# Kernel optimization log

Hardware: AMD Instinct MI355X
Metric: run time of the kernel (lower is better)

The kernel has to match this reference:

```python
import jax, jax.numpy as jnp
import numpy as np

D_MODEL = 2048
N_STATE = 256          # power of two
RANK = 64
LEVELS = int(np.log2(N_STATE))  # 8 butterfly levels
B, S = 4, 4096


def setup_inputs() -> dict:
    key = jax.random.key(0)
    ks = jax.random.split(key, 7)
    u = jax.random.normal(ks[0], (B, S, D_MODEL), dtype=jnp.float32)
    # stacked 2x2 butterfly factors, one per level (orthogonal-ish init)
    A_factors = jax.random.normal(ks[1], (LEVELS, 2, 2), dtype=jnp.float32)
    A_factors = A_factors / jnp.linalg.norm(A_factors, axis=-1, keepdims=True)
    W_b_rank = jax.random.normal(ks[2], (D_MODEL, RANK), dtype=jnp.float32) * (1.0 / np.sqrt(D_MODEL))
    W_b_state = jax.random.normal(ks[3], (RANK, N_STATE), dtype=jnp.float32) * (1.0 / np.sqrt(RANK))
    W_c_rank = jax.random.normal(ks[4], (N_STATE, RANK), dtype=jnp.float32) * (1.0 / np.sqrt(N_STATE))
    W_c_model = jax.random.normal(ks[5], (RANK, D_MODEL), dtype=jnp.float32) * (1.0 / np.sqrt(RANK))
    D_vec = jax.random.normal(ks[6], (D_MODEL,), dtype=jnp.float32) * 0.02
    return {"u": u, "A_factors": A_factors, "W_b_rank": W_b_rank,
            "W_b_state": W_b_state, "W_c_rank": W_c_rank,
            "W_c_model": W_c_model, "D_vec": D_vec}


def _apply_butterfly(state, A_factors):
    # state: [B, S, N]; reshape N into LEVELS axes of size 2 and apply a 2x2
    # factor along each axis (contracting the axis with A's FIRST dim, i.e.
    # x @ A, matching tf.matmul(flattened, factor)).
    b, s, n = state.shape
    x = state.reshape((b, s) + (2,) * LEVELS)
    for lvl in range(LEVELS):
        ax = 2 + lvl
        x = jnp.moveaxis(jnp.tensordot(x, A_factors[lvl], axes=[[ax], [0]]), -1, ax)
    return x.reshape(b, s, n)


def reference(u, A_factors, W_b_rank, W_b_state, W_c_rank, W_c_model, D_vec):
    # B path: low-rank projection to state space
    state = (u @ W_b_rank) @ W_b_state              # [B,S,N]
    # A: butterfly-structured state transform
    state = _apply_butterfly(state, A_factors)      # [B,S,N]
    # C path: low-rank projection back to model dim
    y = (state @ W_c_rank) @ W_c_model              # [B,S,D]
    # D: elementwise feedthrough
    return y + D_vec * u
```

## Files before the change

### kernel.cpp

```cpp
#include <hip/hip_runtime.h>

typedef unsigned short ushort_t;
typedef __attribute__((ext_vector_type(8))) short bf16x8;
typedef __attribute__((ext_vector_type(4))) float f32x4;
typedef __attribute__((ext_vector_type(4))) unsigned short us4;

#define DM 2048
#define RK 64

__device__ __forceinline__ ushort_t f2b(float f) {
    union { float f; unsigned u; } x; x.f = f;
    unsigned r = x.u + 0x7fff + ((x.u >> 16) & 1);
    return (ushort_t)(r >> 16);
}

__global__ void k_p1(const float* __restrict__ Wbs, const float* __restrict__ Af,
                     const float* __restrict__ Wcr, float* __restrict__ Mmid) {
    __shared__ float X[64 * 256];
    const int tid = threadIdx.x;

#pragma unroll
    for (int i = 0; i < 16; ++i) {
        int e = (i * 256 + tid) * 4;
        *(float4*)&X[e] = *(const float4*)&Wbs[e];
    }
    __syncthreads();

#pragma unroll
    for (int l = 0; l < 8; ++l) {
        const int bit = 1 << (7 - l);
        const float a00 = Af[l * 4 + 0], a01 = Af[l * 4 + 1];
        const float a10 = Af[l * 4 + 2], a11 = Af[l * 4 + 3];
#pragma unroll 4
        for (int p = 0; p < 32; ++p) {
            int pid = p * 256 + tid;
            int row = pid >> 7;
            int off = pid & 127;
            int lo = off & (bit - 1);
            int n0 = ((off ^ lo) << 1) | lo;
            int n1 = n0 | bit;
            float x0 = X[row * 256 + n0], x1 = X[row * 256 + n1];
            X[row * 256 + n0] = x0 * a00 + x1 * a10;
            X[row * 256 + n1] = x0 * a01 + x1 * a11;
        }
        __syncthreads();
    }

    int g = blockIdx.x * 256 + tid;
    int r1 = g >> 6, r2 = g & 63;
    float s = 0.f;
#pragma unroll 8
    for (int n = 0; n < 256; ++n) s += X[r1 * 256 + n] * Wcr[n * 64 + r2];
    Mmid[g] = s;
}

__global__ void k_p2(const float* __restrict__ Wbr, const float* __restrict__ Mmid,
                     const float* __restrict__ Wcm,
                     ushort_t* __restrict__ WeffT, ushort_t* __restrict__ WcT) {
    const int b = blockIdx.x, tid = threadIdx.x;
    if (b < 32) {
        __shared__ float LW[64][65];
        __shared__ float LM[64 * 64];
#pragma unroll
        for (int i = 0; i < 4; ++i) {
            int e = (i * 256 + tid) * 4;
            int kk = e >> 6, r = e & 63;
            float4 v = *(const float4*)&Wbr[(size_t)b * 4096 + e];
            LW[kk][r] = v.x; LW[kk][r + 1] = v.y; LW[kk][r + 2] = v.z; LW[kk][r + 3] = v.w;
        }
#pragma unroll
        for (int i = 0; i < 4; ++i) {
            int e = (i * 256 + tid) * 4;
            *(float4*)&LM[e] = *(const float4*)&Mmid[e];
        }
        __syncthreads();

        int kk = tid & 63, n0 = (tid >> 6) * 16;
        float acc[16];
#pragma unroll
        for (int j = 0; j < 16; ++j) acc[j] = 0.f;
        for (int r = 0; r < 64; ++r) {
            float wv = LW[kk][r];
            const float* mrow = &LM[r * 64 + n0];
            float4 m0 = *(const float4*)(mrow);
            float4 m1 = *(const float4*)(mrow + 4);
            float4 m2 = *(const float4*)(mrow + 8);
            float4 m3 = *(const float4*)(mrow + 12);
            acc[0] += wv * m0.x; acc[1] += wv * m0.y; acc[2] += wv * m0.z; acc[3] += wv * m0.w;
            acc[4] += wv * m1.x; acc[5] += wv * m1.y; acc[6] += wv * m1.z; acc[7] += wv * m1.w;
            acc[8] += wv * m2.x; acc[9] += wv * m2.y; acc[10] += wv * m2.z; acc[11] += wv * m2.w;
            acc[12] += wv * m3.x; acc[13] += wv * m3.y; acc[14] += wv * m3.z; acc[15] += wv * m3.w;
        }
#pragma unroll
        for (int j = 0; j < 16; ++j)
            WeffT[(size_t)(n0 + j) * DM + b * 64 + kk] = f2b(acc[j]);
    } else {
        __shared__ float LT[64][65];
        const int n0 = (b - 32) * 64;
#pragma unroll
        for (int i = 0; i < 4; ++i) {
            int e = (i * 256 + tid) * 4;
            int k = e >> 6, nn = e & 63;
            float4 v = *(const float4*)&Wcm[(size_t)k * DM + n0 + nn];
            LT[k][nn] = v.x; LT[k][nn + 1] = v.y; LT[k][nn + 2] = v.z; LT[k][nn + 3] = v.w;
        }
        __syncthreads();
#pragma unroll
        for (int i = 0; i < 4; ++i) {
            int e = (i * 256 + tid) * 4;
            int nn = e >> 6, k = e & 63;
            us4 o;
            o.x = f2b(LT[k][nn]); o.y = f2b(LT[k + 1][nn]);
            o.z = f2b(LT[k + 2][nn]); o.w = f2b(LT[k + 3][nn]);
            *(us4*)&WcT[(size_t)(n0 + nn) * RK + k] = o;
        }
    }
}

__global__ __launch_bounds__(512, 5) void k_main(const float* __restrict__ u,
                                                 const ushort_t* __restrict__ WeffT,
                                                 const ushort_t* __restrict__ WcT,
                                                 const float* __restrict__ Dvec,
                                                 float* __restrict__ out) {
    __shared__ float red[8][64][20];
    __shared__ ushort_t tsh[16 * 72];

    const int tid = threadIdx.x;
    const int w = tid >> 6;
    const int lane = tid & 63;
    const int m16 = lane & 15;
    const int quad = lane >> 4;
    const size_t row0 = (size_t)blockIdx.x * 16;
    const float* ub = u + row0 * DM;

    f32x4 acc0 = {0.f, 0.f, 0.f, 0.f}, acc1 = acc0, acc2 = acc0, acc3 = acc0;
    const float* ap = ub + m16 * DM + w * 256 + quad * 8;
    const ushort_t* bp0 = WeffT + (size_t)m16 * DM + w * 256 + quad * 8;
#pragma unroll 4
    for (int ks = 0; ks < 8; ++ks) {
        const int k0 = ks * 32;
        float4 u0 = *(const float4*)(ap + k0);
        float4 u1 = *(const float4*)(ap + k0 + 4);
        bf16x8 a;
        a[0] = (short)f2b(u0.x); a[1] = (short)f2b(u0.y);
        a[2] = (short)f2b(u0.z); a[3] = (short)f2b(u0.w);
        a[4] = (short)f2b(u1.x); a[5] = (short)f2b(u1.y);
        a[6] = (short)f2b(u1.z); a[7] = (short)f2b(u1.w);
        bf16x8 b0 = *(const bf16x8*)(bp0 + k0);
        bf16x8 b1 = *(const bf16x8*)(bp0 + 16 * DM + k0);
        bf16x8 b2 = *(const bf16x8*)(bp0 + 32 * DM + k0);
        bf16x8 b3 = *(const bf16x8*)(bp0 + 48 * DM + k0);
        acc0 = __builtin_amdgcn_mfma_f32_16x16x32_bf16(a, b0, acc0, 0, 0, 0);
        acc1 = __builtin_amdgcn_mfma_f32_16x16x32_bf16(a, b1, acc1, 0, 0, 0);
        acc2 = __builtin_amdgcn_mfma_f32_16x16x32_bf16(a, b2, acc2, 0, 0, 0);
        acc3 = __builtin_amdgcn_mfma_f32_16x16x32_bf16(a, b3, acc3, 0, 0, 0);
    }
    *(f32x4*)&red[w][ 0 + m16][quad * 4] = acc0;
    *(f32x4*)&red[w][16 + m16][quad * 4] = acc1;
    *(f32x4*)&red[w][32 + m16][quad * 4] = acc2;
    *(f32x4*)&red[w][48 + m16][quad * 4] = acc3;
    __syncthreads();

    {
        const int n = tid >> 3, r2 = (tid & 7) * 2;
        float s0 = 0.f, s1 = 0.f;
#pragma unroll
        for (int ww = 0; ww < 8; ++ww) {
            float2 v = *(const float2*)&red[ww][n][r2];
            s0 += v.x; s1 += v.y;
        }
        tsh[r2 * 72 + n]       = f2b(s0);
        tsh[(r2 + 1) * 72 + n] = f2b(s1);
    }
    __syncthreads();

    bf16x8 ta0 = *(const bf16x8*)&tsh[m16 * 72 + quad * 8];
    bf16x8 ta1 = *(const bf16x8*)&tsh[m16 * 72 + 32 + quad * 8];
    const ushort_t* wcb = WcT + (size_t)(w * 256 + m16) * RK + quad * 8;
    const float* u2 = ub + m16 * DM + w * 256 + quad * 4;
    const float* dp = Dvec + w * 256 + quad * 4;
    float* op = out + (row0 + m16) * DM + w * 256 + quad * 4;
#pragma unroll 2
    for (int nt = 0; nt < 16; ++nt) {
        const ushort_t* bp2 = wcb + nt * 16 * RK;
        bf16x8 wb0 = *(const bf16x8*)(bp2);
        bf16x8 wb1 = *(const bf16x8*)(bp2 + 32);
        f32x4 o = {0.f, 0.f, 0.f, 0.f};
        o = __builtin_amdgcn_mfma_f32_16x16x32_bf16(wb0, ta0, o, 0, 0, 0);
        o = __builtin_amdgcn_mfma_f32_16x16x32_bf16(wb1, ta1, o, 0, 0, 0);
        float4 uv = *(const float4*)(u2 + nt * 16);
        float4 dv = *(const float4*)(dp + nt * 16);
        f32x4 st;
        st.x = o[0] + dv.x * uv.x;
        st.y = o[1] + dv.y * uv.y;
        st.z = o[2] + dv.z * uv.z;
        st.w = o[3] + dv.w * uv.w;
        __builtin_nontemporal_store(st, (f32x4*)(op + nt * 16));
    }
}

extern "C" void kernel_launch(void* const* d_in, const int* in_sizes, int n_in,
                              void* d_out, int out_size, void* d_ws, size_t ws_size,
                              hipStream_t stream) {
    (void)in_sizes; (void)n_in; (void)out_size; (void)ws_size;
    const float* u   = (const float*)d_in[0];
    const float* Af  = (const float*)d_in[1];
    const float* Wbr = (const float*)d_in[2];
    const float* Wbs = (const float*)d_in[3];
    const float* Wcr = (const float*)d_in[4];
    const float* Wcm = (const float*)d_in[5];
    const float* Dv  = (const float*)d_in[6];
    float* out = (float*)d_out;

    char* ws = (char*)d_ws;
    float*    Mmid  = (float*)(ws + 0);
    ushort_t* WeffT = (ushort_t*)(ws + 16384);
    ushort_t* WcT   = (ushort_t*)(ws + 278528);

    k_p1<<<16, 256, 0, stream>>>(Wbs, Af, Wcr, Mmid);
    k_p2<<<64, 256, 0, stream>>>(Wbr, Mmid, Wcm, WeffT, WcT);
    k_main<<<1024, 512, 0, stream>>>(u, WeffT, WcT, Dv, out);
}
```

Before: 327.2 us.

## Split fused main kernel into separate reduce and expand kernels

Splits the fused k_main into two launches. k_a uses 128-thread blocks, each warp covering half of K, and writes the rank-64 intermediate for each 16-row block to global memory as bf16. k_b uses 256-thread blocks that read that intermediate and do the output projection plus the D feedthrough. The aim is to drop the 8-way shared-memory reduction and the large-block occupancy limit. In exchange, u is read twice across two kernels, there is an extra launch, and a global round-trip for the intermediate.

New measurement: 323.1 us. About the same (-1.2%).

```diff
diff --git a/kernel.cpp b/kernel.cpp
--- a/kernel.cpp
+++ b/kernel.cpp
@@ -18,14 +18,12 @@
                      const float* __restrict__ Wcr, float* __restrict__ Mmid) {
     __shared__ float X[64 * 256];
     const int tid = threadIdx.x;
-
 #pragma unroll
     for (int i = 0; i < 16; ++i) {
         int e = (i * 256 + tid) * 4;
         *(float4*)&X[e] = *(const float4*)&Wbs[e];
     }
     __syncthreads();
-
 #pragma unroll
     for (int l = 0; l < 8; ++l) {
         const int bit = 1 << (7 - l);
@@ -45,7 +43,6 @@
         }
         __syncthreads();
     }
-
     int g = blockIdx.x * 256 + tid;
     int r1 = g >> 6, r2 = g & 63;
     float s = 0.f;
@@ -74,7 +71,6 @@
             *(float4*)&LM[e] = *(const float4*)&Mmid[e];
         }
         __syncthreads();
-
         int kk = tid & 63, n0 = (tid >> 6) * 16;
         float acc[16];
 #pragma unroll
@@ -117,28 +113,23 @@
     }
 }
 
-__global__ __launch_bounds__(512, 5) void k_main(const float* __restrict__ u,
-                                                 const ushort_t* __restrict__ WeffT,
-                                                 const ushort_t* __restrict__ WcT,
-                                                 const float* __restrict__ Dvec,
-                                                 float* __restrict__ out) {
-    __shared__ float red[8][64][20];
-    __shared__ ushort_t tsh[16 * 72];
-
+__global__ __launch_bounds__(128) void k_a(const float* __restrict__ u,
+                                           const ushort_t* __restrict__ WeffT,
+                                           ushort_t* __restrict__ tg) {
+    __shared__ float red[2][16][68];
     const int tid = threadIdx.x;
     const int w = tid >> 6;
     const int lane = tid & 63;
     const int m16 = lane & 15;
     const int quad = lane >> 4;
     const size_t row0 = (size_t)blockIdx.x * 16;
-    const float* ub = u + row0 * DM;
+    const float* ap = u + (row0 + m16) * DM + w * 1024 + quad * 8;
+    const ushort_t* bp0 = WeffT + (size_t)m16 * DM + w * 1024 + quad * 8;
 
     f32x4 acc0 = {0.f, 0.f, 0.f, 0.f}, acc1 = acc0, acc2 = acc0, acc3 = acc0;
-    const float* ap = ub + m16 * DM + w * 256 + quad * 8;
-    const ushort_t* bp0 = WeffT + (size_t)m16 * DM + w * 256 + quad * 8;
 #pragma unroll 4
-    for (int ks = 0; ks < 8; ++ks) {
-        const int k0 = ks * 32;
+    for (int kk = 0; kk < 32; ++kk) {
+        const int k0 = kk * 32;
         float4 u0 = *(const float4*)(ap + k0);
         float4 u1 = *(const float4*)(ap + k0 + 4);
         bf16x8 a;
@@ -155,33 +146,53 @@
         acc2 = __builtin_amdgcn_mfma_f32_16x16x32_bf16(a, b2, acc2, 0, 0, 0);
         acc3 = __builtin_amdgcn_mfma_f32_16x16x32_bf16(a, b3, acc3, 0, 0, 0);
     }
-    *(f32x4*)&red[w][ 0 + m16][quad * 4] = acc0;
-    *(f32x4*)&red[w][16 + m16][quad * 4] = acc1;
-    *(f32x4*)&red[w][32 + m16][quad * 4] = acc2;
-    *(f32x4*)&red[w][48 + m16][quad * 4] = acc3;
+#pragma unroll
+    for (int i = 0; i < 4; ++i) {
+        red[w][quad * 4 + i][ 0 + m16] = acc0[i];
+        red[w][quad * 4 + i][16 + m16] = acc1[i];
+        red[w][quad * 4 + i][32 + m16] = acc2[i];
+        red[w][quad * 4 + i][48 + m16] = acc3[i];
+    }
     __syncthreads();
 
     {
-        const int n = tid >> 3, r2 = (tid & 7) * 2;
-        float s0 = 0.f, s1 = 0.f;
-#pragma unroll
-        for (int ww = 0; ww < 8; ++ww) {
-            float2 v = *(const float2*)&red[ww][n][r2];
-            s0 += v.x; s1 += v.y;
-        }
-        tsh[r2 * 72 + n]       = f2b(s0);
-        tsh[(r2 + 1) * 72 + n] = f2b(s1);
-    }
-    __syncthreads();
-
-    bf16x8 ta0 = *(const bf16x8*)&tsh[m16 * 72 + quad * 8];
-    bf16x8 ta1 = *(const bf16x8*)&tsh[m16 * 72 + 32 + quad * 8];
-    const ushort_t* wcb = WcT + (size_t)(w * 256 + m16) * RK + quad * 8;
-    const float* u2 = ub + m16 * DM + w * 256 + quad * 4;
-    const float* dp = Dvec + w * 256 + quad * 4;
-    float* op = out + (row0 + m16) * DM + w * 256 + quad * 4;
+        const int row = tid >> 3, c0 = (tid & 7) * 8;
+        float4 p0 = *(const float4*)&red[0][row][c0];
+        float4 p1 = *(const float4*)&red[0][row][c0 + 4];
+        float4 q0 = *(const float4*)&red[1][row][c0];
+        float4 q1 = *(const float4*)&red[1][row][c0 + 4];
+        us4 o0, o1;
+        o0.x = f2b(p0.x + q0.x); o0.y = f2b(p0.y + q0.y);
+        o0.z = f2b(p0.z + q0.z); o0.w = f2b(p0.w + q0.w);
+        o1.x = f2b(p1.x + q1.x); o1.y = f2b(p1.y + q1.y);
+        o1.z = f2b(p1.z + q1.z); o1.w = f2b(p1.w + q1.w);
+        ushort_t* tp = tg + (size_t)blockIdx.x * 1024 + tid * 8;
+        *(us4*)tp = o0;
+        *(us4*)(tp + 4) = o1;
+    }
+}
+
+__global__ __launch_bounds__(256) void k_b(const ushort_t* __restrict__ tg,
+                                           const float* __restrict__ u,
+                                           const ushort_t* __restrict__ WcT,
+                                           const float* __restrict__ Dvec,
+                                           float* __restrict__ out) {
+    const int tid = threadIdx.x;
+    const int w = tid >> 6;
+    const int lane = tid & 63;
+    const int m16 = lane & 15;
+    const int quad = lane >> 4;
+    const size_t row0 = (size_t)blockIdx.x * 16;
+    const ushort_t* tb = tg + (size_t)blockIdx.x * 1024;
+
+    bf16x8 ta0 = *(const bf16x8*)&tb[m16 * 64 + quad * 8];
+    bf16x8 ta1 = *(const bf16x8*)&tb[m16 * 64 + 32 + quad * 8];
+    const ushort_t* wcb = WcT + (size_t)(w * 512 + m16) * RK + quad * 8;
+    const float* u2 = u + (row0 + m16) * DM + w * 512 + quad * 4;
+    const float* dp = Dvec + w * 512 + quad * 4;
+    float* op = out + (row0 + m16) * DM + w * 512 + quad * 4;
 #pragma unroll 2
-    for (int nt = 0; nt < 16; ++nt) {
+    for (int nt = 0; nt < 32; ++nt) {
         const ushort_t* bp2 = wcb + nt * 16 * RK;
         bf16x8 wb0 = *(const bf16x8*)(bp2);
         bf16x8 wb1 = *(const bf16x8*)(bp2 + 32);
@@ -216,8 +227,10 @@
     float*    Mmid  = (float*)(ws + 0);
     ushort_t* WeffT = (ushort_t*)(ws + 16384);
     ushort_t* WcT   = (ushort_t*)(ws + 278528);
+    ushort_t* tg    = (ushort_t*)(ws + 540672);
 
     k_p1<<<16, 256, 0, stream>>>(Wbs, Af, Wcr, Mmid);
     k_p2<<<64, 256, 0, stream>>>(Wbr, Mmid, Wcm, WeffT, WcT);
-    k_main<<<1024, 512, 0, stream>>>(u, WeffT, WcT, Dv, out);
-}
+    k_a <<<1024, 128, 0, stream>>>(u, WeffT, tg);
+    k_b <<<1024, 256, 0, stream>>>(tg, u, WcT, Dv, out);
+}
```

## Use 4-wave blocks with software-prefetched loads in main fused kernel

Applied to the files above, without the earlier changes.

Halves the block size of the main kernel from 8 to 4 waves, so each wave covers a 512-wide K slice (16 MFMA steps) and a 512-wide output slice. Both loops gain explicit register double-buffering that issues the next iteration's global loads before the current MFMAs. The cross-wave reduction buffer is laid out transposed so the reduction reads contiguous float4 rows. The aim is to hide global-load latency and cut reduction traffic, at the cost of more registers per thread and fewer waves per block to hide latency.

Result: slower. 354.8 us (+8.4%).

```diff
diff --git a/kernel.cpp b/kernel.cpp
--- a/kernel.cpp
+++ b/kernel.cpp
@@ -18,14 +18,12 @@
                      const float* __restrict__ Wcr, float* __restrict__ Mmid) {
     __shared__ float X[64 * 256];
     const int tid = threadIdx.x;
-
 #pragma unroll
     for (int i = 0; i < 16; ++i) {
         int e = (i * 256 + tid) * 4;
         *(float4*)&X[e] = *(const float4*)&Wbs[e];
     }
     __syncthreads();
-
 #pragma unroll
     for (int l = 0; l < 8; ++l) {
         const int bit = 1 << (7 - l);
@@ -45,7 +43,6 @@
         }
         __syncthreads();
     }
-
     int g = blockIdx.x * 256 + tid;
     int r1 = g >> 6, r2 = g & 63;
     float s = 0.f;
@@ -74,7 +71,6 @@
             *(float4*)&LM[e] = *(const float4*)&Mmid[e];
         }
         __syncthreads();
-
         int kk = tid & 63, n0 = (tid >> 6) * 16;
         float acc[16];
 #pragma unroll
@@ -117,12 +113,12 @@
     }
 }
 
-__global__ __launch_bounds__(512, 5) void k_main(const float* __restrict__ u,
+__global__ __launch_bounds__(256, 4) void k_main(const float* __restrict__ u,
                                                  const ushort_t* __restrict__ WeffT,
                                                  const ushort_t* __restrict__ WcT,
                                                  const float* __restrict__ Dvec,
                                                  float* __restrict__ out) {
-    __shared__ float red[8][64][20];
+    __shared__ float red[4][16][68];
     __shared__ ushort_t tsh[16 * 72];
 
     const int tid = threadIdx.x;
@@ -133,69 +129,99 @@
     const size_t row0 = (size_t)blockIdx.x * 16;
     const float* ub = u + row0 * DM;
 
+    const float* ap = ub + m16 * DM + w * 512 + quad * 8;
+    const ushort_t* bp = WeffT + (size_t)m16 * DM + w * 512 + quad * 8;
+
     f32x4 acc0 = {0.f, 0.f, 0.f, 0.f}, acc1 = acc0, acc2 = acc0, acc3 = acc0;
-    const float* ap = ub + m16 * DM + w * 256 + quad * 8;
-    const ushort_t* bp0 = WeffT + (size_t)m16 * DM + w * 256 + quad * 8;
-#pragma unroll 4
-    for (int ks = 0; ks < 8; ++ks) {
-        const int k0 = ks * 32;
-        float4 u0 = *(const float4*)(ap + k0);
-        float4 u1 = *(const float4*)(ap + k0 + 4);
+    float4 u0c = *(const float4*)(ap);
+    float4 u1c = *(const float4*)(ap + 4);
+    bf16x8 b0c = *(const bf16x8*)(bp);
+    bf16x8 b1c = *(const bf16x8*)(bp + 16 * DM);
+    bf16x8 b2c = *(const bf16x8*)(bp + 32 * DM);
+    bf16x8 b3c = *(const bf16x8*)(bp + 48 * DM);
+#pragma unroll
+    for (int kk = 0; kk < 16; ++kk) {
+        float4 u0n, u1n; bf16x8 b0n, b1n, b2n, b3n;
+        if (kk < 15) {
+            const int k0 = (kk + 1) * 32;
+            u0n = *(const float4*)(ap + k0);
+            u1n = *(const float4*)(ap + k0 + 4);
+            b0n = *(const bf16x8*)(bp + k0);
+            b1n = *(const bf16x8*)(bp + 16 * DM + k0);
+            b2n = *(const bf16x8*)(bp + 32 * DM + k0);
+            b3n = *(const bf16x8*)(bp + 48 * DM + k0);
+        }
         bf16x8 a;
-        a[0] = (short)f2b(u0.x); a[1] = (short)f2b(u0.y);
-        a[2] = (short)f2b(u0.z); a[3] = (short)f2b(u0.w);
-        a[4] = (short)f2b(u1.x); a[5] = (short)f2b(u1.y);
-        a[6] = (short)f2b(u1.z); a[7] = (short)f2b(u1.w);
-        bf16x8 b0 = *(const bf16x8*)(bp0 + k0);
-        bf16x8 b1 = *(const bf16x8*)(bp0 + 16 * DM + k0);
-        bf16x8 b2 = *(const bf16x8*)(bp0 + 32 * DM + k0);
-        bf16x8 b3 = *(const bf16x8*)(bp0 + 48 * DM + k0);
-        acc0 = __builtin_amdgcn_mfma_f32_16x16x32_bf16(a, b0, acc0, 0, 0, 0);
-        acc1 = __builtin_amdgcn_mfma_f32_16x16x32_bf16(a, b1, acc1, 0, 0, 0);
-        acc2 = __builtin_amdgcn_mfma_f32_16x16x32_bf16(a, b2, acc2, 0, 0, 0);
-        acc3 = __builtin_amdgcn_mfma_f32_16x16x32_bf16(a, b3, acc3, 0, 0, 0);
-    }
-    *(f32x4*)&red[w][ 0 + m16][quad * 4] = acc0;
-    *(f32x4*)&red[w][16 + m16][quad * 4] = acc1;
-    *(f32x4*)&red[w][32 + m16][quad * 4] = acc2;
-    *(f32x4*)&red[w][48 + m16][quad * 4] = acc3;
+        a[0] = (short)f2b(u0c.x); a[1] = (short)f2b(u0c.y);
+        a[2] = (short)f2b(u0c.z); a[3] = (short)f2b(u0c.w);
+        a[4] = (short)f2b(u1c.x); a[5] = (short)f2b(u1c.y);
+        a[6] = (short)f2b(u1c.z); a[7] = (short)f2b(u1c.w);
+        acc0 = __builtin_amdgcn_mfma_f32_16x16x32_bf16(a, b0c, acc0, 0, 0, 0);
+        acc1 = __builtin_amdgcn_mfma_f32_16x16x32_bf16(a, b1c, acc1, 0, 0, 0);
+        acc2 = __builtin_amdgcn_mfma_f32_16x16x32_bf16(a, b2c, acc2, 0, 0, 0);
+        acc3 = __builtin_amdgcn_mfma_f32_16x16x32_bf16(a, b3c, acc3, 0, 0, 0);
+        if (kk < 15) {
+            u0c = u0n; u1c = u1n;
+            b0c = b0n; b1c = b1n; b2c = b2n; b3c = b3n;
+        }
+    }
+#pragma unroll
+    for (int i = 0; i < 4; ++i) {
+        red[w][quad * 4 + i][ 0 + m16] = acc0[i];
+        red[w][quad * 4 + i][16 + m16] = acc1[i];
+        red[w][quad * 4 + i][32 + m16] = acc2[i];
+        red[w][quad * 4 + i][48 + m16] = acc3[i];
+    }
     __syncthreads();
 
     {
-        const int n = tid >> 3, r2 = (tid & 7) * 2;
-        float s0 = 0.f, s1 = 0.f;
-#pragma unroll
-        for (int ww = 0; ww < 8; ++ww) {
-            float2 v = *(const float2*)&red[ww][n][r2];
-            s0 += v.x; s1 += v.y;
-        }
-        tsh[r2 * 72 + n]       = f2b(s0);
-        tsh[(r2 + 1) * 72 + n] = f2b(s1);
+        const int row = tid >> 4, c0 = (tid & 15) * 4;
+        float4 s0 = *(const float4*)&red[0][row][c0];
+        float4 s1 = *(const float4*)&red[1][row][c0];
+        float4 s2 = *(const float4*)&red[2][row][c0];
+        float4 s3 = *(const float4*)&red[3][row][c0];
+        us4 o;
+        o.x = f2b(s0.x + s1.x + s2.x + s3.x);
+        o.y = f2b(s0.y + s1.y + s2.y + s3.y);
+        o.z = f2b(s0.z + s1.z + s2.z + s3.z);
+        o.w = f2b(s0.w + s1.w + s2.w + s3.w);
+        *(us4*)&tsh[row * 72 + c0] = o;
     }
     __syncthreads();
 
     bf16x8 ta0 = *(const bf16x8*)&tsh[m16 * 72 + quad * 8];
     bf16x8 ta1 = *(const bf16x8*)&tsh[m16 * 72 + 32 + quad * 8];
-    const ushort_t* wcb = WcT + (size_t)(w * 256 + m16) * RK + quad * 8;
-    const float* u2 = ub + m16 * DM + w * 256 + quad * 4;
-    const float* dp = Dvec + w * 256 + quad * 4;
-    float* op = out + (row0 + m16) * DM + w * 256 + quad * 4;
-#pragma unroll 2
-    for (int nt = 0; nt < 16; ++nt) {
-        const ushort_t* bp2 = wcb + nt * 16 * RK;
-        bf16x8 wb0 = *(const bf16x8*)(bp2);
-        bf16x8 wb1 = *(const bf16x8*)(bp2 + 32);
+    const ushort_t* wcb = WcT + (size_t)(w * 512 + m16) * RK + quad * 8;
+    const float* u2 = ub + m16 * DM + w * 512 + quad * 4;
+    const float* dp = Dvec + w * 512 + quad * 4;
+    float* op = out + (row0 + m16) * DM + w * 512 + quad * 4;
+
+    bf16x8 wb0c = *(const bf16x8*)(wcb);
+    bf16x8 wb1c = *(const bf16x8*)(wcb + 32);
+    float4 uvc = *(const float4*)(u2);
+    float4 dvc = *(const float4*)(dp);
+#pragma unroll 4
+    for (int nt = 0; nt < 32; ++nt) {
+        bf16x8 wb0n, wb1n; float4 uvn, dvn;
+        if (nt < 31) {
+            const ushort_t* bp2 = wcb + (nt + 1) * 16 * RK;
+            wb0n = *(const bf16x8*)(bp2);
+            wb1n = *(const bf16x8*)(bp2 + 32);
+            uvn = *(const float4*)(u2 + (nt + 1) * 16);
+            dvn = *(const float4*)(dp + (nt + 1) * 16);
+        }
         f32x4 o = {0.f, 0.f, 0.f, 0.f};
-        o = __builtin_amdgcn_mfma_f32_16x16x32_bf16(wb0, ta0, o, 0, 0, 0);
-        o = __builtin_amdgcn_mfma_f32_16x16x32_bf16(wb1, ta1, o, 0, 0, 0);
-        float4 uv = *(const float4*)(u2 + nt * 16);
-        float4 dv = *(const float4*)(dp + nt * 16);
+        o = __builtin_amdgcn_mfma_f32_16x16x32_bf16(wb0c, ta0, o, 0, 0, 0);
+        o = __builtin_amdgcn_mfma_f32_16x16x32_bf16(wb1c, ta1, o, 0, 0, 0);
         f32x4 st;
-        st.x = o[0] + dv.x * uv.x;
-        st.y = o[1] + dv.y * uv.y;
-        st.z = o[2] + dv.z * uv.z;
-        st.w = o[3] + dv.w * uv.w;
+        st.x = o[0] + dvc.x * uvc.x;
+        st.y = o[1] + dvc.y * uvc.y;
+        st.z = o[2] + dvc.z * uvc.z;
+        st.w = o[3] + dvc.w * uvc.w;
         __builtin_nontemporal_store(st, (f32x4*)(op + nt * 16));
+        if (nt < 31) {
+            wb0c = wb0n; wb1c = wb1n; uvc = uvn; dvc = dvn;
+        }
     }
 }
 
@@ -219,5 +245,5 @@
 
     k_p1<<<16, 256, 0, stream>>>(Wbs, Af, Wcr, Mmid);
     k_p2<<<64, 256, 0, stream>>>(Wbr, Mmid, Wcm, WeffT, WcT);
-    k_main<<<1024, 512, 0, stream>>>(u, WeffT, WcT, Dv, out);
-}
+    k_main<<<1024, 256, 0, stream>>>(u, WeffT, WcT, Dv, out);
+}
```

## Restructure main kernel to single-wave blocks with double-buffered LDS staging of u

Applied to the files above, without the earlier changes.

The main kernel now runs one wavefront per 16-row block instead of eight wavefronts splitting the K dimension. Each wave walks the full 2048-wide K in 16 stages. Tiles of u are staged into a swizzled, double-buffered LDS buffer with global_load_lds, and the cross-wave LDS reduction is removed. The goal is to overlap u loads with MFMA work and drop the reduction and barrier cost. In exchange, each CU gets far fewer waves to hide latency, the output epilogue becomes a 128-iteration serial loop in one wave, and the nontemporal store hint is removed. There is no explicit wait between the LDS DMA loads and the LDS reads, so correctness depends on the waits the compiler inserts.

Result: slower. 337.7 us (+3.2%).

```diff
diff --git a/kernel.cpp b/kernel.cpp
--- a/kernel.cpp
+++ b/kernel.cpp
@@ -18,14 +18,12 @@
                      const float* __restrict__ Wcr, float* __restrict__ Mmid) {
     __shared__ float X[64 * 256];
     const int tid = threadIdx.x;
-
 #pragma unroll
     for (int i = 0; i < 16; ++i) {
         int e = (i * 256 + tid) * 4;
         *(float4*)&X[e] = *(const float4*)&Wbs[e];
     }
     __syncthreads();
-
 #pragma unroll
     for (int l = 0; l < 8; ++l) {
         const int bit = 1 << (7 - l);
@@ -45,7 +43,6 @@
         }
         __syncthreads();
     }
-
     int g = blockIdx.x * 256 + tid;
     int r1 = g >> 6, r2 = g & 63;
     float s = 0.f;
@@ -74,7 +71,6 @@
             *(float4*)&LM[e] = *(const float4*)&Mmid[e];
         }
         __syncthreads();
-
         int kk = tid & 63, n0 = (tid >> 6) * 16;
         float acc[16];
 #pragma unroll
@@ -117,72 +113,87 @@
     }
 }
 
-__global__ __launch_bounds__(512, 5) void k_main(const float* __restrict__ u,
-                                                 const ushort_t* __restrict__ WeffT,
-                                                 const ushort_t* __restrict__ WcT,
-                                                 const float* __restrict__ Dvec,
-                                                 float* __restrict__ out) {
-    __shared__ float red[8][64][20];
+__global__ __launch_bounds__(64, 1) void k_main(const float* __restrict__ u,
+                                                const ushort_t* __restrict__ WeffT,
+                                                const ushort_t* __restrict__ WcT,
+                                                const float* __restrict__ Dvec,
+                                                float* __restrict__ out) {
+    __shared__ float sbuf[2][16 * 128];
     __shared__ ushort_t tsh[16 * 72];
 
-    const int tid = threadIdx.x;
-    const int w = tid >> 6;
-    const int lane = tid & 63;
+    const int lane = threadIdx.x;
     const int m16 = lane & 15;
     const int quad = lane >> 4;
     const size_t row0 = (size_t)blockIdx.x * 16;
     const float* ub = u + row0 * DM;
 
+#define STAGE(BUF, S)                                                          \
+    {                                                                          \
+        _Pragma("unroll")                                                      \
+        for (int j = 0; j < 8; ++j) {                                          \
+            int srow = j * 2 + (lane >> 5);                                    \
+            int p = lane & 31;                                                 \
+            int g = p ^ srow ^ ((srow & 2) << 3);                              \
+            const float* gp = ub + (size_t)srow * DM + (S) * 128 + g * 4;      \
+            __builtin_amdgcn_global_load_lds(                                  \
+                (const __attribute__((address_space(1))) void*)gp,             \
+                (__attribute__((address_space(3))) void*)&sbuf[BUF][j * 256],  \
+                16, 0, 0);                                                     \
+        }                                                                      \
+    }
+
     f32x4 acc0 = {0.f, 0.f, 0.f, 0.f}, acc1 = acc0, acc2 = acc0, acc3 = acc0;
-    const float* ap = ub + m16 * DM + w * 256 + quad * 8;
-    const ushort_t* bp0 = WeffT + (size_t)m16 * DM + w * 256 + quad * 8;
-#pragma unroll 4
-    for (int ks = 0; ks < 8; ++ks) {
-        const int k0 = ks * 32;
-        float4 u0 = *(const float4*)(ap + k0);
-        float4 u1 = *(const float4*)(ap + k0 + 4);
-        bf16x8 a;
-        a[0] = (short)f2b(u0.x); a[1] = (short)f2b(u0.y);
-        a[2] = (short)f2b(u0.z); a[3] = (short)f2b(u0.w);
-        a[4] = (short)f2b(u1.x); a[5] = (short)f2b(u1.y);
-        a[6] = (short)f2b(u1.z); a[7] = (short)f2b(u1.w);
-        bf16x8 b0 = *(const bf16x8*)(bp0 + k0);
-        bf16x8 b1 = *(const bf16x8*)(bp0 + 16 * DM + k0);
-        bf16x8 b2 = *(const bf16x8*)(bp0 + 32 * DM + k0);
-        bf16x8 b3 = *(const bf16x8*)(bp0 + 48 * DM + k0);
-        acc0 = __builtin_amdgcn_mfma_f32_16x16x32_bf16(a, b0, acc0, 0, 0, 0);
-        acc1 = __builtin_amdgcn_mfma_f32_16x16x32_bf16(a, b1, acc1, 0, 0, 0);
-        acc2 = __builtin_amdgcn_mfma_f32_16x16x32_bf16(a, b2, acc2, 0, 0, 0);
-        acc3 = __builtin_amdgcn_mfma_f32_16x16x32_bf16(a, b3, acc3, 0, 0, 0);
-    }
-    *(f32x4*)&red[w][ 0 + m16][quad * 4] = acc0;
-    *(f32x4*)&red[w][16 + m16][quad * 4] = acc1;
-    *(f32x4*)&red[w][32 + m16][quad * 4] = acc2;
-    *(f32x4*)&red[w][48 + m16][quad * 4] = acc3;
-    __syncthreads();
-
-    {
-        const int n = tid >> 3, r2 = (tid & 7) * 2;
-        float s0 = 0.f, s1 = 0.f;
-#pragma unroll
-        for (int ww = 0; ww < 8; ++ww) {
-            float2 v = *(const float2*)&red[ww][n][r2];
-            s0 += v.x; s1 += v.y;
-        }
-        tsh[r2 * 72 + n]       = f2b(s0);
-        tsh[(r2 + 1) * 72 + n] = f2b(s1);
+
+    STAGE(0, 0);
+    for (int s = 0; s < 16; ++s) {
+        const int cur = s & 1;
+        bf16x8 wf0[4], wf1[4], wf2[4], wf3[4];
+#pragma unroll
+        for (int ks = 0; ks < 4; ++ks) {
+            const ushort_t* wp = WeffT + (size_t)m16 * DM + s * 128 + ks * 32 + quad * 8;
+            wf0[ks] = *(const bf16x8*)(wp);
+            wf1[ks] = *(const bf16x8*)(wp + 16 * DM);
+            wf2[ks] = *(const bf16x8*)(wp + 32 * DM);
+            wf3[ks] = *(const bf16x8*)(wp + 48 * DM);
+        }
+        if (s < 15) STAGE(cur ^ 1, s + 1);
+
+#pragma unroll
+        for (int ks = 0; ks < 4; ++ks) {
+            const int c0 = ks * 8 + quad * 2;
+            const int swz = m16 ^ ((m16 & 2) << 3);
+            f32x4 va = *(const f32x4*)&sbuf[cur][m16 * 128 + (c0 ^ swz) * 4];
+            f32x4 vb = *(const f32x4*)&sbuf[cur][m16 * 128 + ((c0 + 1) ^ swz) * 4];
+            bf16x8 a;
+            a[0] = (short)f2b(va[0]); a[1] = (short)f2b(va[1]);
+            a[2] = (short)f2b(va[2]); a[3] = (short)f2b(va[3]);
+            a[4] = (short)f2b(vb[0]); a[5] = (short)f2b(vb[1]);
+            a[6] = (short)f2b(vb[2]); a[7] = (short)f2b(vb[3]);
+            acc0 = __builtin_amdgcn_mfma_f32_16x16x32_bf16(a, wf0[ks], acc0, 0, 0, 0);
+            acc1 = __builtin_amdgcn_mfma_f32_16x16x32_bf16(a, wf1[ks], acc1, 0, 0, 0);
+            acc2 = __builtin_amdgcn_mfma_f32_16x16x32_bf16(a, wf2[ks], acc2, 0, 0, 0);
+            acc3 = __builtin_amdgcn_mfma_f32_16x16x32_bf16(a, wf3[ks], acc3, 0, 0, 0);
+        }
+    }
+
+#pragma unroll
+    for (int i = 0; i < 4; ++i) {
+        tsh[(quad * 4 + i) * 72 +  0 + m16] = f2b(acc0[i]);
+        tsh[(quad * 4 + i) * 72 + 16 + m16] = f2b(acc1[i]);
+        tsh[(quad * 4 + i) * 72 + 32 + m16] = f2b(acc2[i]);
+        tsh[(quad * 4 + i) * 72 + 48 + m16] = f2b(acc3[i]);
     }
     __syncthreads();
 
     bf16x8 ta0 = *(const bf16x8*)&tsh[m16 * 72 + quad * 8];
     bf16x8 ta1 = *(const bf16x8*)&tsh[m16 * 72 + 32 + quad * 8];
-    const ushort_t* wcb = WcT + (size_t)(w * 256 + m16) * RK + quad * 8;
-    const float* u2 = ub + m16 * DM + w * 256 + quad * 4;
-    const float* dp = Dvec + w * 256 + quad * 4;
-    float* op = out + (row0 + m16) * DM + w * 256 + quad * 4;
-#pragma unroll 2
-    for (int nt = 0; nt < 16; ++nt) {
-        const ushort_t* bp2 = wcb + nt * 16 * RK;
+    const ushort_t* wcb = WcT + (size_t)m16 * RK + quad * 8;
+    const float* u2 = ub + m16 * DM + quad * 4;
+    const float* dp = Dvec + quad * 4;
+    float* op = out + (row0 + m16) * DM + quad * 4;
+#pragma unroll 8
+    for (int nt = 0; nt < 128; ++nt) {
+        const ushort_t* bp2 = wcb + (size_t)nt * 16 * RK;
         bf16x8 wb0 = *(const bf16x8*)(bp2);
         bf16x8 wb1 = *(const bf16x8*)(bp2 + 32);
         f32x4 o = {0.f, 0.f, 0.f, 0.f};
@@ -191,12 +202,13 @@
         float4 uv = *(const float4*)(u2 + nt * 16);
         float4 dv = *(const float4*)(dp + nt * 16);
         f32x4 st;
-        st.x = o[0] + dv.x * uv.x;
-        st.y = o[1] + dv.y * uv.y;
-        st.z = o[2] + dv.z * uv.z;
-        st.w = o[3] + dv.w * uv.w;
-        __builtin_nontemporal_store(st, (f32x4*)(op + nt * 16));
-    }
+        st[0] = o[0] + dv.x * uv.x;
+        st[1] = o[1] + dv.y * uv.y;
+        st[2] = o[2] + dv.z * uv.z;
+        st[3] = o[3] + dv.w * uv.w;
+        *(f32x4*)(op + nt * 16) = st;
+    }
+#undef STAGE
 }
 
 extern "C" void kernel_launch(void* const* d_in, const int* in_sizes, int n_in,
@@ -219,5 +231,5 @@
 
     k_p1<<<16, 256, 0, stream>>>(Wbs, Af, Wcr, Mmid);
     k_p2<<<64, 256, 0, stream>>>(Wbr, Mmid, Wcm, WeffT, WcT);
-    k_main<<<1024, 512, 0, stream>>>(u, WeffT, WcT, Dv, out);
-}
+    k_main<<<1024, 64, 0, stream>>>(u, WeffT, WcT, Dv, out);
+}
```
